# Kernel optimization log

Hardware: AMD Instinct MI355X
Metric: run time of the kernel (lower is better)

## Reference

```python
import jax, jax.numpy as jnp
import numpy as np

B, S, H, NH, DIS = 8, 512, 512, 8, 32
HD = H // NH  # head_dim = 64


def setup_inputs() -> dict:
    key = jax.random.key(0)
    ks = jax.random.split(key, 9)
    sc = 0.05
    return {
        "x": jax.random.normal(ks[0], (B, S, H), jnp.float32),
        "rel_distance": jax.random.randint(ks[1], (B, S, 2 * S), 0, DIS, jnp.int64),
        "mask": jnp.zeros((B, S, 2 * S), jnp.bool_),
        "query_pos_embedding": jax.random.normal(ks[2], (DIS, H), jnp.float32) * sc,
        "key_pos_embedding": jax.random.normal(ks[3], (DIS, H), jnp.float32) * sc,
        "value_pos_embedding": jax.random.normal(ks[4], (DIS, H), jnp.float32) * sc,
        "Wq": jax.random.normal(ks[5], (H, H), jnp.float32) * sc,
        "Wk": jax.random.normal(ks[6], (2 * H, H), jnp.float32) * sc,
        "Wv": jax.random.normal(ks[7], (2 * H, H), jnp.float32) * sc,
        "Wo": jax.random.normal(ks[8], (H, H), jnp.float32) * sc,
    }


def reference(x, rel_distance, mask, query_pos_embedding, key_pos_embedding,
              value_pos_embedding, Wq, Wk, Wv, Wo):
    b, s, _ = x.shape
    scale = jnp.sqrt(jnp.asarray(HD, x.dtype))

    # projections (torch Linear: y = x @ W.T)
    q = (x @ Wq.T).reshape(b, s, NH, HD).transpose(0, 2, 1, 3)        # [B,h,S,d]
    k = (x @ Wk.T).reshape(b, 2 * s, NH, HD).transpose(0, 2, 1, 3)    # [B,h,2S,d]
    v = (x @ Wv.T).reshape(b, 2 * s, NH, HD).transpose(0, 2, 1, 3)    # [B,h,2S,d]

    rel = jnp.broadcast_to(rel_distance[:, None], (b, NH, s, 2 * s))  # [B,h,S,2S]

    # relative-position weights via gather along distance axis
    q_emb = query_pos_embedding.reshape(DIS, NH, HD)                  # [n,h,d]
    qpw_full = jnp.einsum('bhsd,nhd->bhsn', q, q_emb)                 # [B,h,S,n]
    qpw = jnp.take_along_axis(qpw_full, rel, axis=3)                  # [B,h,S,2S]

    k_emb = key_pos_embedding.reshape(DIS, NH, HD)
    kpw_full = jnp.einsum('bhkd,nhd->bhkn', k, k_emb)                 # [B,h,2S,n]
    kpw = jnp.take_along_axis(kpw_full, rel.transpose(0, 1, 3, 2), axis=3)  # [B,h,2S,S]
    kpw = kpw.transpose(0, 1, 3, 2)                                   # [B,h,S,2S]

    scores = (jnp.einsum('bhsd,bhkd->bhsk', q, k) + qpw + kpw) / scale
    scores = jnp.where(mask[:, None], -jnp.inf, scores)
    probs = jax.nn.softmax(scores, axis=-1)                           # [B,h,S,2S]

    # scatter-add probs into distance buckets: [B,h,S,n]
    bi = jnp.arange(b)[:, None, None, None]
    hi = jnp.arange(NH)[None, :, None, None]
    si = jnp.arange(s)[None, None, :, None]
    vdw = jnp.zeros((b, NH, s, DIS), probs.dtype).at[bi, hi, si, rel].add(probs)

    v_emb = value_pos_embedding.reshape(DIS, NH, HD)                  # [n,h,d]
    out = jnp.einsum('bhsk,bhkd->bhsd', probs, v) \
        + jnp.einsum('bhsn,nhd->bhsd', vdw, v_emb)                    # [B,h,S,d]
    out = out.transpose(0, 2, 1, 3).reshape(b, s, H)
    return out @ Wo.T
```

## Files before the change

kernel.cpp:

```cpp
#include <hip/hip_runtime.h>
#include <math.h>

#define Bc 8
#define Sc 512
#define Hc 512
#define NHc 8
#define HDc 64
#define DISc 32
#define S2c 1024

typedef __attribute__((ext_vector_type(8))) short bf16x8;
typedef __attribute__((ext_vector_type(4))) float f32x4;
#define MFMA16(a, b, c) __builtin_amdgcn_mfma_f32_16x16x32_bf16(a, b, c, 0, 0, 0)

__device__ __forceinline__ unsigned short f2bf(float f) {
  unsigned u = __float_as_uint(f);
  return (unsigned short)((u + 0x7fffu + ((u >> 16) & 1u)) >> 16);
}
__device__ __forceinline__ float b2f(unsigned short u) {
  return __uint_as_float((unsigned)u << 16);
}
__device__ __forceinline__ bf16x8 ldb16x8(const unsigned short* p) {
  union { uint4 u; bf16x8 s; } cv;
  cv.u = *(const uint4*)p;
  return cv.s;
}

__global__ __launch_bounds__(256) void cvt5_k(
    const float* __restrict__ x, const float* __restrict__ wq,
    const float* __restrict__ wk, const float* __restrict__ wv,
    const float* __restrict__ wo, unsigned short* __restrict__ x16,
    unsigned short* __restrict__ w16q, unsigned short* __restrict__ w16k,
    unsigned short* __restrict__ w16v, unsigned short* __restrict__ w16o) {
  int i = blockIdx.x * 256 + threadIdx.x;
  const float* src; unsigned short* dst; int off; float sc = 1.f;
  if (i < 524288)      { src = x;  dst = x16;  off = i; }
  else if (i < 589824) { src = wq; dst = w16q; off = i - 524288; sc = 0.125f; }
  else if (i < 720896) { src = wk; dst = w16k; off = i - 589824; }
  else if (i < 851968) { src = wv; dst = w16v; off = i - 720896; }
  else                 { src = wo; dst = w16o; off = i - 851968; }
  float4 v = ((const float4*)src)[off];
  ushort4 u;
  u.x = f2bf(v.x * sc); u.y = f2bf(v.y * sc);
  u.z = f2bf(v.z * sc); u.w = f2bf(v.w * sc);
  ((ushort4*)dst)[off] = u;
}

__global__ __launch_bounds__(256) void pack_k(const int* __restrict__ rel,
                                              const unsigned char* __restrict__ mask,
                                              unsigned char* __restrict__ pk8) {
  int i = blockIdx.x * 256 + threadIdx.x;
  const int* rp = rel + i * 16;
  uint4 mu = *(const uint4*)(mask + i * 16);
  const unsigned char* mb = (const unsigned char*)&mu;
  uint4 o;
  unsigned* ow = (unsigned*)&o;
#pragma unroll
  for (int g = 0; g < 4; ++g) {
    int4 r4 = ((const int4*)rp)[g];
    unsigned b0 = ((unsigned)r4.x & 31u) | (mb[g * 4 + 0] ? 0x80u : 0u);
    unsigned b1 = ((unsigned)r4.y & 31u) | (mb[g * 4 + 1] ? 0x80u : 0u);
    unsigned b2 = ((unsigned)r4.z & 31u) | (mb[g * 4 + 2] ? 0x80u : 0u);
    unsigned b3 = ((unsigned)r4.w & 31u) | (mb[g * 4 + 3] ? 0x80u : 0u);
    ow[g] = b0 | (b1 << 8) | (b2 << 16) | (b3 << 24);
  }
  *(uint4*)(pk8 + i * 16) = o;
}

__global__ __launch_bounds__(256) void wemb_k(
    const float* __restrict__ qpe, const float* __restrict__ kpe,
    const float* __restrict__ Wq, const float* __restrict__ Wk,
    unsigned short* __restrict__ wqp, unsigned short* __restrict__ wkp) {
  const int bid = blockIdx.x;
  const int cc = bid & 3, unit = bid >> 2;
  const int c0 = cc << 7;
  const int t = threadIdx.x;
  const float* emb; const float* Wsrc; unsigned short* outp; int rowbase, h;
  if (unit < 8) {
    h = unit; emb = qpe; Wsrc = Wq + (size_t)(h * 64) * 512; outp = wqp; rowbase = h * 32;
  } else {
    int u = unit - 8; int e = u >> 3; h = u & 7;
    emb = kpe; Wsrc = Wk + (size_t)(e * 512 + h * 64) * 512; outp = wkp;
    rowbase = e * 256 + h * 32;
  }
  __shared__ float es[32][65];
  __shared__ float wsh[64][132];
  {
    int n = t >> 3, d4 = (t & 7) << 3;
    float4 v0 = *(const float4*)(emb + (size_t)n * 512 + h * 64 + d4);
    float4 v1 = *(const float4*)(emb + (size_t)n * 512 + h * 64 + d4 + 4);
    *(float4*)&es[n][d4] = v0;
    *(float4*)&es[n][d4 + 4] = v1;
  }
#pragma unroll
  for (int p = 0; p < 8; ++p) {
    int slot = t + (p << 8);
    int d = slot >> 5, c4 = (slot & 31) << 2;
    *(float4*)&wsh[d][c4] = *(const float4*)(Wsrc + (size_t)d * 512 + c0 + c4);
  }
  __syncthreads();
  const int n = t >> 3, cb = (t & 7) << 4;
  float acc[16] = {};
#pragma unroll
  for (int d = 0; d < 64; ++d) {
    float ev = es[n][d];
    float4 w0 = *(const float4*)&wsh[d][cb];
    float4 w1 = *(const float4*)&wsh[d][cb + 4];
    float4 w2 = *(const float4*)&wsh[d][cb + 8];
    float4 w3 = *(const float4*)&wsh[d][cb + 12];
    acc[0] = fmaf(ev, w0.x, acc[0]);   acc[1] = fmaf(ev, w0.y, acc[1]);
    acc[2] = fmaf(ev, w0.z, acc[2]);   acc[3] = fmaf(ev, w0.w, acc[3]);
    acc[4] = fmaf(ev, w1.x, acc[4]);   acc[5] = fmaf(ev, w1.y, acc[5]);
    acc[6] = fmaf(ev, w1.z, acc[6]);   acc[7] = fmaf(ev, w1.w, acc[7]);
    acc[8] = fmaf(ev, w2.x, acc[8]);   acc[9] = fmaf(ev, w2.y, acc[9]);
    acc[10] = fmaf(ev, w2.z, acc[10]); acc[11] = fmaf(ev, w2.w, acc[11]);
    acc[12] = fmaf(ev, w3.x, acc[12]); acc[13] = fmaf(ev, w3.y, acc[13]);
    acc[14] = fmaf(ev, w3.z, acc[14]); acc[15] = fmaf(ev, w3.w, acc[15]);
  }
  unsigned short* orow = outp + (size_t)(rowbase + n) * 512 + c0 + cb;
#pragma unroll
  for (int j = 0; j < 16; ++j) orow[j] = f2bf(acc[j] * 0.125f);
}

template <int MODE>
__global__ __launch_bounds__(256, 4) void gemm16_k(
    const unsigned short* __restrict__ A, const unsigned short* __restrict__ B1,
    const unsigned short* __restrict__ B2, void* __restrict__ out1,
    void* __restrict__ out2, int M, int N, int K, int nsplit) {
  const int t = threadIdx.x;
  const int w = t >> 6, lane = t & 63, ln = lane & 15, qd = lane >> 4;
  const int wm = (w >> 1) << 5, wn = (w & 1) << 5;
  const int m0 = blockIdx.y << 6, n0 = blockIdx.x << 6;
  __shared__ unsigned short As[64 * 72];
  __shared__ unsigned short Bs[64 * 72];
  const bool reg1 = (n0 < nsplit);
  const unsigned short* Bb =
      reg1 ? B1 + (size_t)n0 * K : B2 + (size_t)(n0 - nsplit) * K;
  const int r0 = t >> 3, c8 = (t & 7) << 3;
  const unsigned short* ga = A + (size_t)(m0 + r0) * K + c8;
  const unsigned short* gb = Bb + (size_t)r0 * K + c8;
  const size_t half = (size_t)32 * K;
  uint4 va0 = *(const uint4*)ga, va1 = *(const uint4*)(ga + half);
  uint4 vb0 = *(const uint4*)gb, vb1 = *(const uint4*)(gb + half);
  f32x4 z = {0.f, 0.f, 0.f, 0.f};
  f32x4 acc[2][2] = {{z, z}, {z, z}};
  for (int k0 = 0; k0 < K; k0 += 64) {
    *(uint4*)&As[r0 * 72 + c8] = va0;
    *(uint4*)&As[(r0 + 32) * 72 + c8] = va1;
    *(uint4*)&Bs[r0 * 72 + c8] = vb0;
    *(uint4*)&Bs[(r0 + 32) * 72 + c8] = vb1;
    __syncthreads();
    if (k0 + 64 < K) {
      va0 = *(const uint4*)(ga + k0 + 64);
      va1 = *(const uint4*)(ga + half + k0 + 64);
      vb0 = *(const uint4*)(gb + k0 + 64);
      vb1 = *(const uint4*)(gb + half + k0 + 64);
    }
#pragma unroll
    for (int kk = 0; kk < 64; kk += 32) {
      bf16x8 a0 = ldb16x8(&As[(wm + ln) * 72 + kk + qd * 8]);
      bf16x8 a1 = ldb16x8(&As[(wm + 16 + ln) * 72 + kk + qd * 8]);
      bf16x8 b0 = ldb16x8(&Bs[(wn + ln) * 72 + kk + qd * 8]);
      bf16x8 b1 = ldb16x8(&Bs[(wn + 16 + ln) * 72 + kk + qd * 8]);
      acc[0][0] = MFMA16(a0, b0, acc[0][0]);
      acc[0][1] = MFMA16(a0, b1, acc[0][1]);
      acc[1][0] = MFMA16(a1, b0, acc[1][0]);
      acc[1][1] = MFMA16(a1, b1, acc[1][1]);
    }
    __syncthreads();
  }
#pragma unroll
  for (int tm = 0; tm < 2; ++tm)
#pragma unroll
    for (int tn = 0; tn < 2; ++tn)
#pragma unroll
      for (int r = 0; r < 4; ++r) {
        int m = m0 + wm + tm * 16 + qd * 4 + r;
        int n = n0 + wn + tn * 16 + ln;
        float v = acc[tm][tn][r];
        int bb = m >> 9, s = m & 511;
        if (MODE == 0) {
          ((float*)out1)[(size_t)m * N + n] = v;
        } else if (MODE == 3) {
          int e = n >> 9, hh = (n >> 6) & 7, d = n & 63;
          int k2 = 2 * s + e;
          ((unsigned short*)out1)[((size_t)(bb * 8 + hh) * 64 + d) * 1024 + k2] = f2bf(v);
        } else if (MODE == 1) {
          if (reg1) {
            int hh = (n >> 6) & 7, d = n & 63;
            ((unsigned short*)out1)[((size_t)(bb * 8 + hh) * 512 + s) * 64 + d] = f2bf(v);
          } else {
            int n2 = n - 512, hh = n2 >> 5, nn = n2 & 31;
            ((unsigned short*)out2)[((size_t)(bb * 8 + hh) * 512 + s) * 32 + nn] = f2bf(v);
          }
        } else {
          if (reg1) {
            int e = n >> 9, hh = (n >> 6) & 7, d = n & 63;
            int k2 = 2 * s + e;
            ((unsigned short*)out1)[((size_t)(bb * 8 + hh) * 1024 + k2) * 64 + d] = f2bf(v);
          } else {
            int n2 = n - 1024, e = n2 >> 8, hh = (n2 >> 5) & 7, nn = n2 & 31;
            int k2 = 2 * s + e;
            ((unsigned short*)out2)[((size_t)(bb * 8 + hh) * 1024 + k2) * 32 + nn] = f2bf(v);
          }
        }
      }
}

__global__ __launch_bounds__(512, 4) void attn6_k(
    const unsigned short* __restrict__ q16h, const unsigned short* __restrict__ kb16,
    const unsigned short* __restrict__ vT16, const unsigned short* __restrict__ qpw16,
    const unsigned short* __restrict__ kpw16, const unsigned char* __restrict__ pk8,
    const float* __restrict__ v_emb, unsigned short* __restrict__ attn16) {
  const int bid = blockIdx.x;
  const int b = bid & 7;
  const int h = (bid >> 3) & 7;
  const int qb = ((bid >> 6) & 7) << 6;
  const int t = threadIdx.x;
  const int w = t >> 6;
  const int g = w >> 2;
  const int ws4 = w & 3;
  const int lane = t & 63;
  const int ln = lane & 15;
  const int qd = lane >> 4;

  __shared__ __align__(16) char smem[60928];
  unsigned char*  pkt  = (unsigned char*)smem;
  unsigned short* kpws = (unsigned short*)(smem + 10240);
  unsigned short* q32s = (unsigned short*)(smem + 19456);
  unsigned short* pbuf = (unsigned short*)(smem + 24064);
  unsigned long long* vdwm64 = (unsigned long long*)(smem + 42496);
  float*          accbuf = (float*)smem;
  unsigned short* vest   = (unsigned short*)(smem + 24064);
  unsigned short* vdwb   = (unsigned short*)(smem + 29184);

  for (int i = t; i < 4 * 16 * 36; i += 512) vdwm64[i] = 0ull;
  if (t < 256) {
    int row = t >> 2, c8 = (t & 3) << 3;
    *(uint4*)&q32s[row * 36 + c8] =
        *(const uint4*)(qpw16 + ((size_t)((b * 8 + h) * 512 + qb) + row) * 32 + c8);
  }
  const unsigned short* kbase = kb16 + (size_t)(b * 8 + h) * 65536;
  const unsigned short* vbase = vT16 + (size_t)(b * 8 + h) * 65536;
  bf16x8 aQ[2];
  {
    const unsigned short* qsrc =
        q16h + ((size_t)((b * 8 + h) * 512 + qb + ws4 * 16 + ln)) * 64;
    aQ[0] = ldb16x8(qsrc + qd * 8);
    aQ[1] = ldb16x8(qsrc + 32 + qd * 8);
  }
  f32x4 z = {0.f, 0.f, 0.f, 0.f};
  f32x4 acc[4] = {z, z, z, z};

  const int u = t & 255, gg = t >> 8;
  const int qr = u >> 2, cg = (u & 3) << 4;
  const int kc8 = (u & 3) << 3;
  const unsigned char* pks = pk8 + ((size_t)(b * 512 + qb + qr)) * 1024 + (gg << 9);
  const unsigned short* kps =
      kpw16 + ((size_t)((b * 8 + h) * 1024) + (gg << 9) + qr) * 32 + kc8;
  unsigned char* pt_w = pkt + gg * 5120 + qr * 80 + cg;
  unsigned short* kp_w = kpws + gg * 2304 + qr * 36 + kc8;

  uint4 pv = *(const uint4*)(pks + cg);
  uint4 kv = *(const uint4*)kps;

  for (int kti = 0; kti < 8; ++kti) {
    *(uint4*)pt_w = pv;
    *(uint4*)kp_w = kv;
    __syncthreads();
    if (kti < 7) {
      pv = *(const uint4*)(pks + ((kti + 1) << 6) + cg);
      kv = *(const uint4*)(kps + ((size_t)(kti + 1) << 11));
    }
    const int kt0 = (kti + g * 8) << 6;

    f32x4 sc4[4];
#pragma unroll
    for (int t4 = 0; t4 < 4; ++t4) {
      f32x4 c = z;
      c = MFMA16(aQ[0], ldb16x8(kbase + (size_t)(kt0 + t4 * 16 + ln) * 64 + qd * 8), c);
      c = MFMA16(aQ[1], ldb16x8(kbase + (size_t)(kt0 + t4 * 16 + ln) * 64 + 32 + qd * 8), c);
      sc4[t4] = c;
    }

    unsigned char* pt_ = pkt + g * 5120;
    unsigned short* kp_ = kpws + g * 2304;
#pragma unroll
    for (int r = 0; r < 4; ++r) {
#pragma unroll
      for (int t4 = 0; t4 < 4; ++t4) {
        int row_l = ws4 * 16 + qd * 4 + r;
        int kl = t4 * 16 + ln;
        unsigned um = pt_[row_l * 80 + kl];
        int rd = um & 31;
        float s = sc4[t4][r] + b2f(q32s[row_l * 36 + rd]) + b2f(kp_[kl * 36 + rd]);
        float p = (um & 0x80u) ? 0.f : __expf(s);
        atomicAdd(&vdwm64[ws4 * 576 + (qd * 4 + r) * 36 + rd],
                  (unsigned long long)(p * 67108864.0f));
        pbuf[w * 1152 + (qd * 4 + r) * 72 + kl] = f2bf(p);
      }
    }

    bf16x8 a0 = ldb16x8(&pbuf[w * 1152 + ln * 72 + qd * 8]);
    bf16x8 a1 = ldb16x8(&pbuf[w * 1152 + ln * 72 + 32 + qd * 8]);
#pragma unroll
    for (int dt = 0; dt < 4; ++dt) {
      acc[dt] = MFMA16(a0, ldb16x8(vbase + (size_t)(dt * 16 + ln) * 1024 + kt0 + qd * 8), acc[dt]);
      acc[dt] = MFMA16(a1, ldb16x8(vbase + (size_t)(dt * 16 + ln) * 1024 + kt0 + 32 + qd * 8), acc[dt]);
    }
    __syncthreads();
  }

  if (t < 256) {
    int n = t >> 3, d0 = (t & 7) << 3;
    const float* src = v_emb + ((size_t)n << 9) + (h << 6) + d0;
    float4 f0 = *(const float4*)src;
    float4 f1 = *(const float4*)(src + 4);
    vest[(d0 + 0) * 40 + n] = f2bf(f0.x); vest[(d0 + 1) * 40 + n] = f2bf(f0.y);
    vest[(d0 + 2) * 40 + n] = f2bf(f0.z); vest[(d0 + 3) * 40 + n] = f2bf(f0.w);
    vest[(d0 + 4) * 40 + n] = f2bf(f1.x); vest[(d0 + 5) * 40 + n] = f2bf(f1.y);
    vest[(d0 + 6) * 40 + n] = f2bf(f1.z); vest[(d0 + 7) * 40 + n] = f2bf(f1.w);
  } else {
    int row = lane >> 2, n0 = (lane & 3) << 3;
    float vv[8];
#pragma unroll
    for (int j = 0; j < 8; ++j)
      vv[j] = (float)vdwm64[ws4 * 576 + row * 36 + n0 + j] * 1.4901161193847656e-8f;
    ushort4 u0, u1;
    u0.x = f2bf(vv[0]); u0.y = f2bf(vv[1]); u0.z = f2bf(vv[2]); u0.w = f2bf(vv[3]);
    u1.x = f2bf(vv[4]); u1.y = f2bf(vv[5]); u1.z = f2bf(vv[6]); u1.w = f2bf(vv[7]);
    *(ushort4*)&vdwb[ws4 * 640 + row * 40 + n0] = u0;
    *(ushort4*)&vdwb[ws4 * 640 + row * 40 + n0 + 4] = u1;
  }
  __syncthreads();

  if (g == 1) {
    bf16x8 av = ldb16x8(&vdwb[ws4 * 640 + ln * 40 + qd * 8]);
#pragma unroll
    for (int dt = 0; dt < 4; ++dt)
      acc[dt] = MFMA16(av, ldb16x8(&vest[(dt * 16 + ln) * 40 + qd * 8]), acc[dt]);
#pragma unroll
    for (int r = 0; r < 4; ++r)
#pragma unroll
      for (int dt = 0; dt < 4; ++dt)
        accbuf[ws4 * 1088 + (qd * 4 + r) * 68 + dt * 16 + ln] = acc[dt][r];
  }
  __syncthreads();

  if (g == 0) {
    float inv[4];
#pragma unroll
    for (int r = 0; r < 4; ++r) {
      unsigned long long lu = 0ull;
#pragma unroll
      for (int n = 0; n < 32; ++n)
        lu += vdwm64[ws4 * 576 + (qd * 4 + r) * 36 + n];
      inv[r] = 67108864.0f / (float)lu;
    }
    unsigned short* obase =
        attn16 + ((size_t)(b * 512 + qb + ws4 * 16 + qd * 4)) * 512 + (h << 6);
#pragma unroll
    for (int r = 0; r < 4; ++r)
#pragma unroll
      for (int dt = 0; dt < 4; ++dt) {
        float v = (acc[dt][r] + accbuf[ws4 * 1088 + (qd * 4 + r) * 68 + dt * 16 + ln]) * inv[r];
        obase[(size_t)r * 512 + dt * 16 + ln] = f2bf(v);
      }
  }
}

extern "C" void kernel_launch(void* const* d_in, const int* in_sizes, int n_in,
                              void* d_out, int out_size, void* d_ws, size_t ws_size,
                              hipStream_t stream) {
  const float* x = (const float*)d_in[0];
  const int* rel = (const int*)d_in[1];
  const unsigned char* mask = (const unsigned char*)d_in[2];
  const float* qpe = (const float*)d_in[3];
  const float* kpe = (const float*)d_in[4];
  const float* vpe = (const float*)d_in[5];
  const float* Wq = (const float*)d_in[6];
  const float* Wk = (const float*)d_in[7];
  const float* Wv = (const float*)d_in[8];
  const float* Wo = (const float*)d_in[9];
  float* out = (float*)d_out;

  unsigned short* u = (unsigned short*)d_ws;
  unsigned short* x16    = u;
  unsigned short* w16q   = x16 + 2097152;
  unsigned short* w16k   = w16q + 262144;
  unsigned short* w16v   = w16k + 524288;
  unsigned short* w16o   = w16v + 524288;
  unsigned short* wqp16  = w16o + 262144;
  unsigned short* wkp16  = wqp16 + 131072;
  unsigned short* q16h   = wkp16 + 262144;
  unsigned short* qpw16  = q16h + 2097152;
  unsigned short* kb16   = qpw16 + 1048576;
  unsigned short* kpw16  = kb16 + 4194304;
  unsigned short* vT16   = kpw16 + 2097152;
  unsigned short* attn16 = vT16 + 4194304;
  unsigned char* pk8 = (unsigned char*)(attn16 + 2097152);

  pack_k<<<1024, 256, 0, stream>>>(rel, mask, pk8);
  cvt5_k<<<3584, 256, 0, stream>>>(x, Wq, Wk, Wv, Wo, x16, w16q, w16k, w16v, w16o);
  wemb_k<<<96, 256, 0, stream>>>(qpe, kpe, Wq, Wk, wqp16, wkp16);
  gemm16_k<1><<<dim3(12, 64), 256, 0, stream>>>(x16, w16q, wqp16, q16h, qpw16,
                                                4096, 768, 512, 512);
  gemm16_k<2><<<dim3(24, 64), 256, 0, stream>>>(x16, w16k, wkp16, kb16, kpw16,
                                                4096, 1536, 512, 1024);
  gemm16_k<3><<<dim3(16, 64), 256, 0, stream>>>(x16, w16v, nullptr, vT16, nullptr,
                                                4096, 1024, 512, 1024);
  attn6_k<<<512, 512, 0, stream>>>(q16h, kb16, vT16, qpw16, kpw16, pk8, vpe, attn16);
  gemm16_k<0><<<dim3(8, 64), 256, 0, stream>>>(attn16, w16o, nullptr, out, nullptr,
                                               4096, 512, 512, 512);
}
```

Baseline: 220.8 us.

## Merge prep kernels and projection GEMMs, shrink attention histogram to 32-bit atomics

```diff
diff --git a/kernel.cpp b/kernel.cpp
--- a/kernel.cpp
+++ b/kernel.cpp
@@ -1,13 +1,5 @@
 #include <hip/hip_runtime.h>
 #include <math.h>
-
-#define Bc 8
-#define Sc 512
-#define Hc 512
-#define NHc 8
-#define HDc 64
-#define DISc 32
-#define S2c 1024
 
 typedef __attribute__((ext_vector_type(8))) short bf16x8;
 typedef __attribute__((ext_vector_type(4))) float f32x4;
@@ -26,131 +18,135 @@
   return cv.s;
 }
 
-__global__ __launch_bounds__(256) void cvt5_k(
-    const float* __restrict__ x, const float* __restrict__ wq,
-    const float* __restrict__ wk, const float* __restrict__ wv,
-    const float* __restrict__ wo, unsigned short* __restrict__ x16,
+__global__ __launch_bounds__(256) void prep_k(
+    const float* __restrict__ x, const int* __restrict__ rel,
+    const unsigned char* __restrict__ mask, const float* __restrict__ qpe,
+    const float* __restrict__ kpe, const float* __restrict__ Wq,
+    const float* __restrict__ Wk, const float* __restrict__ Wv,
+    const float* __restrict__ Wo, unsigned short* __restrict__ x16,
     unsigned short* __restrict__ w16q, unsigned short* __restrict__ w16k,
-    unsigned short* __restrict__ w16v, unsigned short* __restrict__ w16o) {
-  int i = blockIdx.x * 256 + threadIdx.x;
-  const float* src; unsigned short* dst; int off; float sc = 1.f;
-  if (i < 524288)      { src = x;  dst = x16;  off = i; }
-  else if (i < 589824) { src = wq; dst = w16q; off = i - 524288; sc = 0.125f; }
-  else if (i < 720896) { src = wk; dst = w16k; off = i - 589824; }
-  else if (i < 851968) { src = wv; dst = w16v; off = i - 720896; }
-  else                 { src = wo; dst = w16o; off = i - 851968; }
-  float4 v = ((const float4*)src)[off];
-  ushort4 u;
-  u.x = f2bf(v.x * sc); u.y = f2bf(v.y * sc);
-  u.z = f2bf(v.z * sc); u.w = f2bf(v.w * sc);
-  ((ushort4*)dst)[off] = u;
-}
-
-__global__ __launch_bounds__(256) void pack_k(const int* __restrict__ rel,
-                                              const unsigned char* __restrict__ mask,
-                                              unsigned char* __restrict__ pk8) {
-  int i = blockIdx.x * 256 + threadIdx.x;
-  const int* rp = rel + i * 16;
-  uint4 mu = *(const uint4*)(mask + i * 16);
-  const unsigned char* mb = (const unsigned char*)&mu;
-  uint4 o;
-  unsigned* ow = (unsigned*)&o;
-#pragma unroll
-  for (int g = 0; g < 4; ++g) {
-    int4 r4 = ((const int4*)rp)[g];
-    unsigned b0 = ((unsigned)r4.x & 31u) | (mb[g * 4 + 0] ? 0x80u : 0u);
-    unsigned b1 = ((unsigned)r4.y & 31u) | (mb[g * 4 + 1] ? 0x80u : 0u);
-    unsigned b2 = ((unsigned)r4.z & 31u) | (mb[g * 4 + 2] ? 0x80u : 0u);
-    unsigned b3 = ((unsigned)r4.w & 31u) | (mb[g * 4 + 3] ? 0x80u : 0u);
-    ow[g] = b0 | (b1 << 8) | (b2 << 16) | (b3 << 24);
-  }
-  *(uint4*)(pk8 + i * 16) = o;
-}
-
-__global__ __launch_bounds__(256) void wemb_k(
-    const float* __restrict__ qpe, const float* __restrict__ kpe,
-    const float* __restrict__ Wq, const float* __restrict__ Wk,
-    unsigned short* __restrict__ wqp, unsigned short* __restrict__ wkp) {
-  const int bid = blockIdx.x;
-  const int cc = bid & 3, unit = bid >> 2;
-  const int c0 = cc << 7;
-  const int t = threadIdx.x;
-  const float* emb; const float* Wsrc; unsigned short* outp; int rowbase, h;
-  if (unit < 8) {
-    h = unit; emb = qpe; Wsrc = Wq + (size_t)(h * 64) * 512; outp = wqp; rowbase = h * 32;
+    unsigned short* __restrict__ w16v, unsigned short* __restrict__ w16o,
+    unsigned short* __restrict__ wqp, unsigned short* __restrict__ wkp,
+    unsigned char* __restrict__ pk8) {
+  const int bid = blockIdx.x, t = threadIdx.x;
+  if (bid < 3584) {
+    int i = bid * 256 + t;
+    const float* src; unsigned short* dst; int off; float sc = 1.f;
+    if (i < 524288)      { src = x;  dst = x16;  off = i; }
+    else if (i < 589824) { src = Wq; dst = w16q; off = i - 524288; sc = 0.125f; }
+    else if (i < 720896) { src = Wk; dst = w16k; off = i - 589824; }
+    else if (i < 851968) { src = Wv; dst = w16v; off = i - 720896; }
+    else                 { src = Wo; dst = w16o; off = i - 851968; }
+    float4 v = ((const float4*)src)[off];
+    ushort4 u;
+    u.x = f2bf(v.x * sc); u.y = f2bf(v.y * sc);
+    u.z = f2bf(v.z * sc); u.w = f2bf(v.w * sc);
+    ((ushort4*)dst)[off] = u;
+  } else if (bid < 4608) {
+    int i = (bid - 3584) * 256 + t;
+    const int* rp = rel + i * 16;
+    uint4 mu = *(const uint4*)(mask + i * 16);
+    const unsigned char* mb = (const unsigned char*)&mu;
+    uint4 o;
+    unsigned* ow = (unsigned*)&o;
+#pragma unroll
+    for (int g = 0; g < 4; ++g) {
+      int4 r4 = ((const int4*)rp)[g];
+      unsigned b0 = ((unsigned)r4.x & 31u) | (mb[g * 4 + 0] ? 0x80u : 0u);
+      unsigned b1 = ((unsigned)r4.y & 31u) | (mb[g * 4 + 1] ? 0x80u : 0u);
+      unsigned b2 = ((unsigned)r4.z & 31u) | (mb[g * 4 + 2] ? 0x80u : 0u);
+      unsigned b3 = ((unsigned)r4.w & 31u) | (mb[g * 4 + 3] ? 0x80u : 0u);
+      ow[g] = b0 | (b1 << 8) | (b2 << 16) | (b3 << 24);
+    }
+    *(uint4*)(pk8 + i * 16) = o;
   } else {
-    int u = unit - 8; int e = u >> 3; h = u & 7;
-    emb = kpe; Wsrc = Wk + (size_t)(e * 512 + h * 64) * 512; outp = wkp;
-    rowbase = e * 256 + h * 32;
-  }
-  __shared__ float es[32][65];
-  __shared__ float wsh[64][132];
-  {
-    int n = t >> 3, d4 = (t & 7) << 3;
-    float4 v0 = *(const float4*)(emb + (size_t)n * 512 + h * 64 + d4);
-    float4 v1 = *(const float4*)(emb + (size_t)n * 512 + h * 64 + d4 + 4);
-    *(float4*)&es[n][d4] = v0;
-    *(float4*)&es[n][d4 + 4] = v1;
-  }
-#pragma unroll
-  for (int p = 0; p < 8; ++p) {
-    int slot = t + (p << 8);
-    int d = slot >> 5, c4 = (slot & 31) << 2;
-    *(float4*)&wsh[d][c4] = *(const float4*)(Wsrc + (size_t)d * 512 + c0 + c4);
-  }
-  __syncthreads();
-  const int n = t >> 3, cb = (t & 7) << 4;
-  float acc[16] = {};
-#pragma unroll
-  for (int d = 0; d < 64; ++d) {
-    float ev = es[n][d];
-    float4 w0 = *(const float4*)&wsh[d][cb];
-    float4 w1 = *(const float4*)&wsh[d][cb + 4];
-    float4 w2 = *(const float4*)&wsh[d][cb + 8];
-    float4 w3 = *(const float4*)&wsh[d][cb + 12];
-    acc[0] = fmaf(ev, w0.x, acc[0]);   acc[1] = fmaf(ev, w0.y, acc[1]);
-    acc[2] = fmaf(ev, w0.z, acc[2]);   acc[3] = fmaf(ev, w0.w, acc[3]);
-    acc[4] = fmaf(ev, w1.x, acc[4]);   acc[5] = fmaf(ev, w1.y, acc[5]);
-    acc[6] = fmaf(ev, w1.z, acc[6]);   acc[7] = fmaf(ev, w1.w, acc[7]);
-    acc[8] = fmaf(ev, w2.x, acc[8]);   acc[9] = fmaf(ev, w2.y, acc[9]);
-    acc[10] = fmaf(ev, w2.z, acc[10]); acc[11] = fmaf(ev, w2.w, acc[11]);
-    acc[12] = fmaf(ev, w3.x, acc[12]); acc[13] = fmaf(ev, w3.y, acc[13]);
-    acc[14] = fmaf(ev, w3.z, acc[14]); acc[15] = fmaf(ev, w3.w, acc[15]);
-  }
-  unsigned short* orow = outp + (size_t)(rowbase + n) * 512 + c0 + cb;
-#pragma unroll
-  for (int j = 0; j < 16; ++j) orow[j] = f2bf(acc[j] * 0.125f);
-}
-
-template <int MODE>
-__global__ __launch_bounds__(256, 4) void gemm16_k(
-    const unsigned short* __restrict__ A, const unsigned short* __restrict__ B1,
-    const unsigned short* __restrict__ B2, void* __restrict__ out1,
-    void* __restrict__ out2, int M, int N, int K, int nsplit) {
+    int bid2 = bid - 4608;
+    int cc = bid2 & 7, unit = bid2 >> 3;
+    int c0 = cc << 6;
+    const float* emb; const float* Wsrc; unsigned short* outp; int rowbase, h;
+    if (unit < 8) {
+      h = unit; emb = qpe; Wsrc = Wq + (size_t)(h * 64) * 512; outp = wqp;
+      rowbase = h * 32;
+    } else {
+      int uu = unit - 8; int e = uu >> 3; h = uu & 7;
+      emb = kpe; Wsrc = Wk + (size_t)(e * 512 + h * 64) * 512; outp = wkp;
+      rowbase = e * 256 + h * 32;
+    }
+    __shared__ float es[32][65];
+    __shared__ float wsh[64][68];
+    {
+      int n = t >> 3, d4 = (t & 7) << 3;
+      float4 v0 = *(const float4*)(emb + (size_t)n * 512 + h * 64 + d4);
+      float4 v1 = *(const float4*)(emb + (size_t)n * 512 + h * 64 + d4 + 4);
+      *(float4*)&es[n][d4] = v0;
+      *(float4*)&es[n][d4 + 4] = v1;
+    }
+#pragma unroll
+    for (int p = 0; p < 4; ++p) {
+      int slot = t + (p << 8);
+      int d = slot >> 4, c4 = (slot & 15) << 2;
+      *(float4*)&wsh[d][c4] = *(const float4*)(Wsrc + (size_t)d * 512 + c0 + c4);
+    }
+    __syncthreads();
+    const int n = t >> 3, cb = (t & 7) << 3;
+    float acc[8] = {};
+#pragma unroll
+    for (int d = 0; d < 64; ++d) {
+      float ev = es[n][d];
+      float4 w0 = *(const float4*)&wsh[d][cb];
+      float4 w1 = *(const float4*)&wsh[d][cb + 4];
+      acc[0] = fmaf(ev, w0.x, acc[0]); acc[1] = fmaf(ev, w0.y, acc[1]);
+      acc[2] = fmaf(ev, w0.z, acc[2]); acc[3] = fmaf(ev, w0.w, acc[3]);
+      acc[4] = fmaf(ev, w1.x, acc[4]); acc[5] = fmaf(ev, w1.y, acc[5]);
+      acc[6] = fmaf(ev, w1.z, acc[6]); acc[7] = fmaf(ev, w1.w, acc[7]);
+    }
+    unsigned short* orow = outp + (size_t)(rowbase + n) * 512 + c0 + cb;
+#pragma unroll
+    for (int j = 0; j < 8; ++j) orow[j] = f2bf(acc[j] * 0.125f);
+  }
+}
+
+__global__ __launch_bounds__(256, 4) void projgemm_k(
+    const unsigned short* __restrict__ A, const unsigned short* __restrict__ w16q,
+    const unsigned short* __restrict__ wqp, const unsigned short* __restrict__ w16k,
+    const unsigned short* __restrict__ wkp, const unsigned short* __restrict__ w16v,
+    unsigned short* __restrict__ q16h, unsigned short* __restrict__ qpw16,
+    unsigned short* __restrict__ kb16, unsigned short* __restrict__ kpw16,
+    unsigned short* __restrict__ vT16) {
   const int t = threadIdx.x;
   const int w = t >> 6, lane = t & 63, ln = lane & 15, qd = lane >> 4;
   const int wm = (w >> 1) << 5, wn = (w & 1) << 5;
-  const int m0 = blockIdx.y << 6, n0 = blockIdx.x << 6;
-  __shared__ unsigned short As[64 * 72];
-  __shared__ unsigned short Bs[64 * 72];
-  const bool reg1 = (n0 < nsplit);
-  const unsigned short* Bb =
-      reg1 ? B1 + (size_t)n0 * K : B2 + (size_t)(n0 - nsplit) * K;
+  const int m0 = blockIdx.y << 6;
+  const int nx = blockIdx.x;
+  int mode, n0;
+  const unsigned short* Bb;
+  if (nx < 12) {
+    mode = 1; n0 = nx << 6;
+    Bb = (n0 < 512) ? w16q + (size_t)n0 * 512 : wqp + (size_t)(n0 - 512) * 512;
+  } else if (nx < 36) {
+    mode = 2; n0 = (nx - 12) << 6;
+    Bb = (n0 < 1024) ? w16k + (size_t)n0 * 512 : wkp + (size_t)(n0 - 1024) * 512;
+  } else {
+    mode = 3; n0 = (nx - 36) << 6;
+    Bb = w16v + (size_t)n0 * 512;
+  }
+  __shared__ unsigned short As[64 * 76];
+  __shared__ unsigned short Bs[64 * 76];
   const int r0 = t >> 3, c8 = (t & 7) << 3;
-  const unsigned short* ga = A + (size_t)(m0 + r0) * K + c8;
-  const unsigned short* gb = Bb + (size_t)r0 * K + c8;
-  const size_t half = (size_t)32 * K;
+  const unsigned short* ga = A + (size_t)(m0 + r0) * 512 + c8;
+  const unsigned short* gb = Bb + (size_t)r0 * 512 + c8;
+  const size_t half = (size_t)32 * 512;
   uint4 va0 = *(const uint4*)ga, va1 = *(const uint4*)(ga + half);
   uint4 vb0 = *(const uint4*)gb, vb1 = *(const uint4*)(gb + half);
   f32x4 z = {0.f, 0.f, 0.f, 0.f};
   f32x4 acc[2][2] = {{z, z}, {z, z}};
-  for (int k0 = 0; k0 < K; k0 += 64) {
-    *(uint4*)&As[r0 * 72 + c8] = va0;
-    *(uint4*)&As[(r0 + 32) * 72 + c8] = va1;
-    *(uint4*)&Bs[r0 * 72 + c8] = vb0;
-    *(uint4*)&Bs[(r0 + 32) * 72 + c8] = vb1;
-    __syncthreads();
-    if (k0 + 64 < K) {
+  for (int k0 = 0; k0 < 512; k0 += 64) {
+    *(uint4*)&As[r0 * 76 + c8] = va0;
+    *(uint4*)&As[(r0 + 32) * 76 + c8] = va1;
+    *(uint4*)&Bs[r0 * 76 + c8] = vb0;
+    *(uint4*)&Bs[(r0 + 32) * 76 + c8] = vb1;
+    __syncthreads();
+    if (k0 + 64 < 512) {
       va0 = *(const uint4*)(ga + k0 + 64);
       va1 = *(const uint4*)(ga + half + k0 + 64);
       vb0 = *(const uint4*)(gb + k0 + 64);
@@ -158,10 +154,10 @@
     }
 #pragma unroll
     for (int kk = 0; kk < 64; kk += 32) {
-      bf16x8 a0 = ldb16x8(&As[(wm + ln) * 72 + kk + qd * 8]);
-      bf16x8 a1 = ldb16x8(&As[(wm + 16 + ln) * 72 + kk + qd * 8]);
-      bf16x8 b0 = ldb16x8(&Bs[(wn + ln) * 72 + kk + qd * 8]);
-      bf16x8 b1 = ldb16x8(&Bs[(wn + 16 + ln) * 72 + kk + qd * 8]);
+      bf16x8 a0 = ldb16x8(&As[(wm + ln) * 76 + kk + qd * 8]);
+      bf16x8 a1 = ldb16x8(&As[(wm + 16 + ln) * 76 + kk + qd * 8]);
+      bf16x8 b0 = ldb16x8(&Bs[(wn + ln) * 76 + kk + qd * 8]);
+      bf16x8 b1 = ldb16x8(&Bs[(wn + 16 + ln) * 76 + kk + qd * 8]);
       acc[0][0] = MFMA16(a0, b0, acc[0][0]);
       acc[0][1] = MFMA16(a0, b1, acc[0][1]);
       acc[1][0] = MFMA16(a1, b0, acc[1][0]);
@@ -179,35 +175,87 @@
         int n = n0 + wn + tn * 16 + ln;
         float v = acc[tm][tn][r];
         int bb = m >> 9, s = m & 511;
-        if (MODE == 0) {
-          ((float*)out1)[(size_t)m * N + n] = v;
-        } else if (MODE == 3) {
-          int e = n >> 9, hh = (n >> 6) & 7, d = n & 63;
-          int k2 = 2 * s + e;
-          ((unsigned short*)out1)[((size_t)(bb * 8 + hh) * 64 + d) * 1024 + k2] = f2bf(v);
-        } else if (MODE == 1) {
-          if (reg1) {
+        if (mode == 1) {
+          if (n < 512) {
             int hh = (n >> 6) & 7, d = n & 63;
-            ((unsigned short*)out1)[((size_t)(bb * 8 + hh) * 512 + s) * 64 + d] = f2bf(v);
+            q16h[((size_t)(bb * 8 + hh) * 512 + s) * 64 + d] = f2bf(v);
           } else {
             int n2 = n - 512, hh = n2 >> 5, nn = n2 & 31;
-            ((unsigned short*)out2)[((size_t)(bb * 8 + hh) * 512 + s) * 32 + nn] = f2bf(v);
+            qpw16[((size_t)(bb * 8 + hh) * 512 + s) * 32 + nn] = f2bf(v);
           }
-        } else {
-          if (reg1) {
+        } else if (mode == 2) {
+          if (n < 1024) {
             int e = n >> 9, hh = (n >> 6) & 7, d = n & 63;
             int k2 = 2 * s + e;
-            ((unsigned short*)out1)[((size_t)(bb * 8 + hh) * 1024 + k2) * 64 + d] = f2bf(v);
+            kb16[((size_t)(bb * 8 + hh) * 1024 + k2) * 64 + d] = f2bf(v);
           } else {
             int n2 = n - 1024, e = n2 >> 8, hh = (n2 >> 5) & 7, nn = n2 & 31;
             int k2 = 2 * s + e;
-            ((unsigned short*)out2)[((size_t)(bb * 8 + hh) * 1024 + k2) * 32 + nn] = f2bf(v);
+            kpw16[((size_t)(bb * 8 + hh) * 1024 + k2) * 32 + nn] = f2bf(v);
           }
+        } else {
+          int e = n >> 9, hh = (n >> 6) & 7, d = n & 63;
+          int k2 = 2 * s + e;
+          vT16[((size_t)(bb * 8 + hh) * 64 + d) * 1024 + k2] = f2bf(v);
         }
       }
 }
 
-__global__ __launch_bounds__(512, 4) void attn6_k(
+__global__ __launch_bounds__(256, 4) void ogemm_k(
+    const unsigned short* __restrict__ A, const unsigned short* __restrict__ B,
+    float* __restrict__ C) {
+  const int t = threadIdx.x;
+  const int w = t >> 6, lane = t & 63, ln = lane & 15, qd = lane >> 4;
+  const int wm = (w >> 1) << 5, wn = (w & 1) << 5;
+  const int m0 = blockIdx.y << 6, n0 = blockIdx.x << 6;
+  __shared__ unsigned short As[64 * 76];
+  __shared__ unsigned short Bs[64 * 76];
+  const int r0 = t >> 3, c8 = (t & 7) << 3;
+  const unsigned short* ga = A + (size_t)(m0 + r0) * 512 + c8;
+  const unsigned short* gb = B + (size_t)(n0 + r0) * 512 + c8;
+  const size_t half = (size_t)32 * 512;
+  uint4 va0 = *(const uint4*)ga, va1 = *(const uint4*)(ga + half);
+  uint4 vb0 = *(const uint4*)gb, vb1 = *(const uint4*)(gb + half);
+  f32x4 z = {0.f, 0.f, 0.f, 0.f};
+  f32x4 acc[2][2] = {{z, z}, {z, z}};
+  for (int k0 = 0; k0 < 512; k0 += 64) {
+    *(uint4*)&As[r0 * 76 + c8] = va0;
+    *(uint4*)&As[(r0 + 32) * 76 + c8] = va1;
+    *(uint4*)&Bs[r0 * 76 + c8] = vb0;
+    *(uint4*)&Bs[(r0 + 32) * 76 + c8] = vb1;
+    __syncthreads();
+    if (k0 + 64 < 512) {
+      va0 = *(const uint4*)(ga + k0 + 64);
+      va1 = *(const uint4*)(ga + half + k0 + 64);
+      vb0 = *(const uint4*)(gb + k0 + 64);
+      vb1 = *(const uint4*)(gb + half + k0 + 64);
+    }
+#pragma unroll
+    for (int kk = 0; kk < 64; kk += 32) {
+      bf16x8 a0 = ldb16x8(&As[(wm + ln) * 76 + kk + qd * 8]);
+      bf16x8 a1 = ldb16x8(&As[(wm + 16 + ln) * 76 + kk + qd * 8]);
+      bf16x8 b0 = ldb16x8(&Bs[(wn + ln) * 76 + kk + qd * 8]);
+      bf16x8 b1 = ldb16x8(&Bs[(wn + 16 + ln) * 76 + kk + qd * 8]);
+      acc[0][0] = MFMA16(a0, b0, acc[0][0]);
+      acc[0][1] = MFMA16(a0, b1, acc[0][1]);
+      acc[1][0] = MFMA16(a1, b0, acc[1][0]);
+      acc[1][1] = MFMA16(a1, b1, acc[1][1]);
+    }
+    __syncthreads();
+  }
+#pragma unroll
+  for (int tm = 0; tm < 2; ++tm)
+#pragma unroll
+    for (int tn = 0; tn < 2; ++tn)
+#pragma unroll
+      for (int r = 0; r < 4; ++r) {
+        int m = m0 + wm + tm * 16 + qd * 4 + r;
+        int n = n0 + wn + tn * 16 + ln;
+        C[(size_t)m * 512 + n] = acc[tm][tn][r];
+      }
+}
+
+__global__ __launch_bounds__(512, 6) void attn7_k(
     const unsigned short* __restrict__ q16h, const unsigned short* __restrict__ kb16,
     const unsigned short* __restrict__ vT16, const unsigned short* __restrict__ qpw16,
     const unsigned short* __restrict__ kpw16, const unsigned char* __restrict__ pk8,
@@ -217,24 +265,20 @@
   const int h = (bid >> 3) & 7;
   const int qb = ((bid >> 6) & 7) << 6;
   const int t = threadIdx.x;
-  const int w = t >> 6;
-  const int g = w >> 2;
-  const int ws4 = w & 3;
-  const int lane = t & 63;
-  const int ln = lane & 15;
-  const int qd = lane >> 4;
-
-  __shared__ __align__(16) char smem[60928];
+  const int w = t >> 6, g = w >> 2, ws4 = w & 3;
+  const int lane = t & 63, ln = lane & 15, qd = lane >> 4;
+
+  __shared__ __align__(16) char smem[49920];
   unsigned char*  pkt  = (unsigned char*)smem;
   unsigned short* kpws = (unsigned short*)(smem + 10240);
   unsigned short* q32s = (unsigned short*)(smem + 19456);
   unsigned short* pbuf = (unsigned short*)(smem + 24064);
-  unsigned long long* vdwm64 = (unsigned long long*)(smem + 42496);
+  unsigned*       vdwm = (unsigned*)(smem + 41472);
   float*          accbuf = (float*)smem;
   unsigned short* vest   = (unsigned short*)(smem + 24064);
   unsigned short* vdwb   = (unsigned short*)(smem + 29184);
 
-  for (int i = t; i < 4 * 16 * 36; i += 512) vdwm64[i] = 0ull;
+  for (int i = t; i < 4 * 16 * 33; i += 512) vdwm[i] = 0u;
   if (t < 256) {
     int row = t >> 2, c8 = (t & 3) << 3;
     *(uint4*)&q32s[row * 36 + c8] =
@@ -295,14 +339,14 @@
         int rd = um & 31;
         float s = sc4[t4][r] + b2f(q32s[row_l * 36 + rd]) + b2f(kp_[kl * 36 + rd]);
         float p = (um & 0x80u) ? 0.f : __expf(s);
-        atomicAdd(&vdwm64[ws4 * 576 + (qd * 4 + r) * 36 + rd],
-                  (unsigned long long)(p * 67108864.0f));
-        pbuf[w * 1152 + (qd * 4 + r) * 72 + kl] = f2bf(p);
+        atomicAdd(&vdwm[ws4 * 528 + (qd * 4 + r) * 33 + rd],
+                  (unsigned)(p * 4096.0f));
+        pbuf[w * 1088 + (qd * 4 + r) * 68 + kl] = f2bf(p);
       }
     }
 
-    bf16x8 a0 = ldb16x8(&pbuf[w * 1152 + ln * 72 + qd * 8]);
-    bf16x8 a1 = ldb16x8(&pbuf[w * 1152 + ln * 72 + 32 + qd * 8]);
+    bf16x8 a0 = ldb16x8(&pbuf[w * 1088 + ln * 68 + qd * 8]);
+    bf16x8 a1 = ldb16x8(&pbuf[w * 1088 + ln * 68 + 32 + qd * 8]);
 #pragma unroll
     for (int dt = 0; dt < 4; ++dt) {
       acc[dt] = MFMA16(a0, ldb16x8(vbase + (size_t)(dt * 16 + ln) * 1024 + kt0 + qd * 8), acc[dt]);
@@ -325,7 +369,7 @@
     float vv[8];
 #pragma unroll
     for (int j = 0; j < 8; ++j)
-      vv[j] = (float)vdwm64[ws4 * 576 + row * 36 + n0 + j] * 1.4901161193847656e-8f;
+      vv[j] = (float)vdwm[ws4 * 528 + row * 33 + n0 + j] * (1.0f / 4096.0f);
     ushort4 u0, u1;
     u0.x = f2bf(vv[0]); u0.y = f2bf(vv[1]); u0.z = f2bf(vv[2]); u0.w = f2bf(vv[3]);
     u1.x = f2bf(vv[4]); u1.y = f2bf(vv[5]); u1.z = f2bf(vv[6]); u1.w = f2bf(vv[7]);
@@ -354,8 +398,8 @@
       unsigned long long lu = 0ull;
 #pragma unroll
       for (int n = 0; n < 32; ++n)
-        lu += vdwm64[ws4 * 576 + (qd * 4 + r) * 36 + n];
-      inv[r] = 67108864.0f / (float)lu;
+        lu += vdwm[ws4 * 528 + (qd * 4 + r) * 33 + n];
+      inv[r] = 4096.0f / (float)lu;
     }
     unsigned short* obase =
         attn16 + ((size_t)(b * 512 + qb + ws4 * 16 + qd * 4)) * 512 + (h << 6);
@@ -400,16 +444,10 @@
   unsigned short* attn16 = vT16 + 4194304;
   unsigned char* pk8 = (unsigned char*)(attn16 + 2097152);
 
-  pack_k<<<1024, 256, 0, stream>>>(rel, mask, pk8);
-  cvt5_k<<<3584, 256, 0, stream>>>(x, Wq, Wk, Wv, Wo, x16, w16q, w16k, w16v, w16o);
-  wemb_k<<<96, 256, 0, stream>>>(qpe, kpe, Wq, Wk, wqp16, wkp16);
-  gemm16_k<1><<<dim3(12, 64), 256, 0, stream>>>(x16, w16q, wqp16, q16h, qpw16,
-                                                4096, 768, 512, 512);
-  gemm16_k<2><<<dim3(24, 64), 256, 0, stream>>>(x16, w16k, wkp16, kb16, kpw16,
-                                                4096, 1536, 512, 1024);
-  gemm16_k<3><<<dim3(16, 64), 256, 0, stream>>>(x16, w16v, nullptr, vT16, nullptr,
-                                                4096, 1024, 512, 1024);
-  attn6_k<<<512, 512, 0, stream>>>(q16h, kb16, vT16, qpw16, kpw16, pk8, vpe, attn16);
-  gemm16_k<0><<<dim3(8, 64), 256, 0, stream>>>(attn16, w16o, nullptr, out, nullptr,
-                                               4096, 512, 512, 512);
-}
+  prep_k<<<4800, 256, 0, stream>>>(x, rel, mask, qpe, kpe, Wq, Wk, Wv, Wo,
+                                   x16, w16q, w16k, w16v, w16o, wqp16, wkp16, pk8);
+  projgemm_k<<<dim3(52, 64), 256, 0, stream>>>(x16, w16q, wqp16, w16k, wkp16, w16v,
+                                               q16h, qpw16, kb16, kpw16, vT16);
+  attn7_k<<<512, 512, 0, stream>>>(q16h, kb16, vT16, qpw16, kpw16, pk8, vpe, attn16);
+  ogemm_k<<<dim3(8, 64), 256, 0, stream>>>(attn16, w16o, out);
+}
```

After: 316.4 us. 1.43x slower.
